# Performance work log

Hardware: AMD Instinct MI355X
Metric: run time of the kernel (lower is better)

Reference implementation:

```python
import jax, jax.numpy as jnp
import numpy as np

B, S, D, E, K = 4, 4096, 1024, 8, 2


def setup_inputs() -> dict:
    key = jax.random.key(0)
    k0, k1, k2 = jax.random.split(key, 3)
    return {
        "x": jax.random.normal(k0, (B, S, D), dtype=jnp.float32),
        "gate_w": jax.random.normal(k1, (E, D), dtype=jnp.float32) * 0.02,   # torch Linear weight [out,in]
        "gate_b": jnp.zeros((E,), dtype=jnp.float32),
        "expert_w": jax.random.normal(k2, (E, D, D), dtype=jnp.float32) * 0.02,  # [E, out, in]
        "expert_b": jnp.zeros((E, D), dtype=jnp.float32),
    }


def reference(x, gate_w, gate_b, expert_w, expert_b):
    b, s, d = x.shape
    h = x.reshape(-1, d)                                   # [T, D], T = b*s
    # Router: gate linear -> softmax (float32) -> top-k -> renormalize
    router_logits = h @ gate_w.T + gate_b                  # [T, E]
    probs = jax.nn.softmax(router_logits.astype(jnp.float32), axis=-1)
    router_weights, selected_experts = jax.lax.top_k(probs, K)  # [T, K]
    router_weights = router_weights / router_weights.sum(axis=-1, keepdims=True)
    router_weights = router_weights.astype(h.dtype)
    # Combine weights per (token, expert): sum of top-k weights routed to each expert
    cw = (jax.nn.one_hot(selected_experts, E, dtype=h.dtype)
          * router_weights[..., None]).sum(axis=1)         # [T, E]
    # Dense-equivalent of gather-linear-scatter: every expert on every token,
    # then weighted combine (mathematically identical to the per-expert loop).
    expert_out = jnp.einsum('td,eod->teo', h, expert_w) + expert_b[None]  # [T, E, D]
    out = jnp.einsum('te,teo->to', cw, expert_out)         # [T, D]
    return out.reshape(b, s, d), router_logits, selected_experts
```

## Files before the change

### kernel.cpp

```cpp
#include <hip/hip_runtime.h>
#include <hip/hip_bf16.h>

#define T_TOK 16384
#define D_DIM 1024
#define E_EXP 8
#define NPAIR 28

#define BM 128
#define BN 64
#define BK 64

#define CNT_STRIDE 64

typedef __attribute__((ext_vector_type(4))) float f32x4;
typedef __attribute__((ext_vector_type(2))) float f32x2;
typedef __attribute__((ext_vector_type(8))) short bf16x8;
typedef __attribute__((ext_vector_type(4))) unsigned short u16x4;

static __device__ __forceinline__ unsigned short f2bf(float f) {
    unsigned int u = __float_as_uint(f);
    unsigned int r = 0x7FFFu + ((u >> 16) & 1u);
    return (unsigned short)((u + r) >> 16);
}

#define GLOAD_LDS16(gp, lp) \
    __builtin_amdgcn_global_load_lds( \
        (const __attribute__((address_space(1))) void*)(gp), \
        (__attribute__((address_space(3))) void*)(lp), 16, 0, 0)

#define RTOK 64
#define RBLK 256
#define CBLK 128
__global__ __launch_bounds__(512) void fused_router_kernel(
    const float* __restrict__ x, const float* __restrict__ gate_w,
    const float* __restrict__ gate_b, float* __restrict__ out_logits,
    float* __restrict__ out_sel, int* __restrict__ counts,
    int* __restrict__ pair_token, f32x2* __restrict__ pair_w,
    unsigned short* __restrict__ xbf,
    const float* __restrict__ expert_w, unsigned short* __restrict__ wbf) {
    const int tid = threadIdx.x;
    if (blockIdx.x >= RBLK) {
        const int b = blockIdx.x - RBLK;
        const int n4 = (E_EXP * D_DIM * D_DIM) / 4;
        for (int i = b * 512 + tid; i < n4; i += CBLK * 512) {
            f32x4 v = ((const f32x4*)expert_w)[i];
            u16x4 p;
            p[0] = f2bf(v[0]); p[1] = f2bf(v[1]); p[2] = f2bf(v[2]); p[3] = f2bf(v[3]);
            ((u16x4*)wbf)[i] = p;
        }
        return;
    }
    __shared__ float gw[E_EXP][D_DIM];
    __shared__ float gb_s[E_EXP];
    __shared__ float logits_s[RTOK][E_EXP];
    __shared__ int   cnt_local[NPAIR];
    __shared__ int   gbase[NPAIR];
    __shared__ int   ent_p[RTOK];
    __shared__ int   ent_pos[RTOK];
    __shared__ f32x2 ent_w[RTOK];

    for (int i = tid; i < E_EXP * D_DIM; i += 512) gw[0][i] = gate_w[i];
    if (tid < E_EXP) gb_s[tid] = gate_b[tid];
    if (tid < NPAIR) cnt_local[tid] = 0;
    __syncthreads();

    const int lane = tid & 63, wv = tid >> 6;
    for (int j = 0; j < RTOK / 8; ++j) {
        const int jt = wv * (RTOK / 8) + j;
        const int t = blockIdx.x * RTOK + jt;
        const float* xrow = x + (size_t)t * D_DIM;
        unsigned short* xbrow = xbf + (size_t)t * D_DIM;
        float acc[E_EXP] = {};
        #pragma unroll
        for (int c = 0; c < 4; ++c) {
            const int col = c * 256 + lane * 4;
            f32x4 xv = *(const f32x4*)(xrow + col);
            u16x4 pk;
            pk[0] = f2bf(xv[0]); pk[1] = f2bf(xv[1]); pk[2] = f2bf(xv[2]); pk[3] = f2bf(xv[3]);
            *(u16x4*)(xbrow + col) = pk;
            #pragma unroll
            for (int e = 0; e < E_EXP; ++e) {
                f32x4 gv = *(const f32x4*)(&gw[e][col]);
                acc[e] += xv[0] * gv[0] + xv[1] * gv[1] + xv[2] * gv[2] + xv[3] * gv[3];
            }
        }
        #pragma unroll
        for (int e = 0; e < E_EXP; ++e) {
            float v = acc[e];
            #pragma unroll
            for (int off = 32; off > 0; off >>= 1) v += __shfl_xor(v, off, 64);
            acc[e] = v;
        }
        if (lane == 0) {
            #pragma unroll
            for (int e = 0; e < E_EXP; ++e) logits_s[jt][e] = acc[e] + gb_s[e];
        }
    }
    __syncthreads();
    if (tid < RTOK) {
        const int t = blockIdx.x * RTOK + tid;
        float l[E_EXP], p[E_EXP];
        float m = -1e30f;
        #pragma unroll
        for (int e = 0; e < E_EXP; ++e) { l[e] = logits_s[tid][e]; m = fmaxf(m, l[e]); }
        float s = 0.f;
        #pragma unroll
        for (int e = 0; e < E_EXP; ++e) { p[e] = expf(l[e] - m); s += p[e]; }
        #pragma unroll
        for (int e = 0; e < E_EXP; ++e) p[e] /= s;
        int e0 = 0; float p0 = p[0];
        #pragma unroll
        for (int e = 1; e < E_EXP; ++e) if (p[e] > p0) { p0 = p[e]; e0 = e; }
        int e1 = -1; float p1 = -1e30f;
        #pragma unroll
        for (int e = 0; e < E_EXP; ++e) if (e != e0 && p[e] > p1) { p1 = p[e]; e1 = e; }
        float denom = p0 + p1;
        float w0 = p0 / denom, w1 = p1 / denom;
        out_sel[t * 2 + 0] = (float)e0;
        out_sel[t * 2 + 1] = (float)e1;
        int lo = min(e0, e1), hi = max(e0, e1);
        float wl = (e0 < e1) ? w0 : w1;
        float wh = (e0 < e1) ? w1 : w0;
        int pp = (lo * (15 - lo)) / 2 + (hi - lo - 1);
        int pos = atomicAdd(&cnt_local[pp], 1);
        ent_p[tid] = pp; ent_pos[tid] = pos;
        f32x2 wv2; wv2[0] = wl; wv2[1] = wh;
        ent_w[tid] = wv2;
    }
    __syncthreads();
    if (tid < NPAIR) gbase[tid] = atomicAdd(&counts[tid * CNT_STRIDE], cnt_local[tid]);
    if (tid < RTOK * E_EXP / 4) {
        f32x4 v = ((const f32x4*)&logits_s[0][0])[tid];
        ((f32x4*)(out_logits + (size_t)blockIdx.x * RTOK * E_EXP))[tid] = v;
    }
    __syncthreads();
    if (tid < RTOK) {
        int pp = ent_p[tid];
        int pos = gbase[pp] + ent_pos[tid];
        pair_token[pp * T_TOK + pos] = blockIdx.x * RTOK + tid;
        pair_w[pp * T_TOK + pos] = ent_w[tid];
    }
}

__global__ __launch_bounds__(256, 2) void moe_gemm_kernel(
    const unsigned short* __restrict__ xbf, const unsigned short* __restrict__ wbf,
    const float* __restrict__ expert_b, const int* __restrict__ counts,
    const int* __restrict__ pair_token, const f32x2* __restrict__ pair_w,
    float* __restrict__ out) {
    const int flat = blockIdx.x;
    const int cls = flat & 7;
    const int nt  = (flat >> 3) & 15;
    const int sup = flat >> 7;

    __shared__ int hdr[5];
    const int tid = threadIdx.x;
    if (tid < 64) {
        int c = (tid < NPAIR) ? counts[tid * CNT_STRIDE] : 0;
        int ntp = (c + BM - 1) >> 7;
        int s = ntp;
        #pragma unroll
        for (int off = 1; off < 64; off <<= 1) {
            int v = __shfl_up(s, off, 64);
            if (tid >= off) s += v;
        }
        int excl = s - ntp;
        int ntot = __shfl(s, NPAIR - 1, 64);
        int chunk = (ntot + 7) >> 3;
        int gidx = cls * chunk + sup;
        bool valid = (sup < chunk) && (gidx < ntot);
        bool mine = valid && (tid < NPAIR) && (gidx >= excl) && (gidx < s);
        unsigned long long mb = __ballot(mine);
        int p = mb ? (__ffsll((long long)mb) - 1) : 0;
        int exclp = __shfl(excl, p, 64);
        int cp = __shfl(c, p, 64);
        if (tid == 0) {
            if (mb == 0) { hdr[0] = -1; }
            else {
                int lo = 0, q = p;
                while (q >= 7 - lo) { q -= 7 - lo; ++lo; }
                hdr[0] = lo; hdr[1] = lo + 1 + q;
                hdr[2] = (gidx - exclp) * BM; hdr[3] = cp; hdr[4] = p;
            }
        }
    }
    __syncthreads();
    const int lo = hdr[0];
    if (lo < 0) return;
    const int hi = hdr[1];
    const int m_base = hdr[2];
    const int cnt = hdr[3];
    const int p = hdr[4];
    const int n_base = nt * BN;

    __shared__ unsigned short As[BM * BK];
    __shared__ unsigned short B0s[BN * BK];
    __shared__ unsigned short B1s[BN * BK];
    __shared__ int tok_s[BM];
    __shared__ f32x2 w_s[BM];

    if (tid < BM) {
        int m = m_base + tid;
        int mc = (m < cnt) ? m : (cnt - 1);
        tok_s[tid] = pair_token[p * T_TOK + mc];
        w_s[tid]   = pair_w[p * T_TOK + mc];
    }
    __syncthreads();

    const int lane = tid & 63;
    const int w = tid >> 6;
    const int lr = lane & 15, lk = lane >> 4;
    const int wm = w >> 1, wn = w & 1;

    const int srow = lane >> 3;
    const int scol = 8 * ((lane & 7) ^ srow);
    const unsigned short* wb0 = wbf + ((size_t)lo << 20);
    const unsigned short* wb1 = wbf + ((size_t)hi << 20);
    const unsigned short* agp[4];
    const unsigned short* b0gp[2];
    const unsigned short* b1gp[2];
    int loffA[4], loffB[2];
    #pragma unroll
    for (int i = 0; i < 4; ++i) {
        int R = i * 32 + w * 8 + srow;
        agp[i]  = xbf + (size_t)tok_s[R] * D_DIM + scol;
        loffA[i] = (i * 32 + w * 8) * BK;
    }
    #pragma unroll
    for (int i = 0; i < 2; ++i) {
        int R = i * 32 + w * 8 + srow;
        b0gp[i] = wb0 + (size_t)(n_base + R) * D_DIM + scol;
        b1gp[i] = wb1 + (size_t)(n_base + R) * D_DIM + scol;
        loffB[i] = (i * 32 + w * 8) * BK;
    }

    f32x4 acc0[4][2] = {};
    f32x4 acc1[4][2] = {};

    for (int k0 = 0; k0 < D_DIM; k0 += BK) {
        #pragma unroll
        for (int i = 0; i < 4; ++i) GLOAD_LDS16(agp[i] + k0, &As[loffA[i]]);
        #pragma unroll
        for (int i = 0; i < 2; ++i) {
            GLOAD_LDS16(b0gp[i] + k0, &B0s[loffB[i]]);
            GLOAD_LDS16(b1gp[i] + k0, &B1s[loffB[i]]);
        }
        __syncthreads();
        #pragma unroll
        for (int kk = 0; kk < 2; ++kk) {
            bf16x8 a[4], b[2], c[2];
            #pragma unroll
            for (int m = 0; m < 4; ++m) {
                int R = wm * 64 + m * 16 + lr;
                int cb = (kk * 64 + lk * 16) ^ ((R & 7) << 4);
                a[m] = *(const bf16x8*)((const char*)As + R * 128 + cb);
            }
            #pragma unroll
            for (int n = 0; n < 2; ++n) {
                int R = wn * 32 + n * 16 + lr;
                int cb = (kk * 64 + lk * 16) ^ ((R & 7) << 4);
                b[n] = *(const bf16x8*)((const char*)B0s + R * 128 + cb);
                c[n] = *(const bf16x8*)((const char*)B1s + R * 128 + cb);
            }
            #pragma unroll
            for (int m = 0; m < 4; ++m)
                #pragma unroll
                for (int n = 0; n < 2; ++n)
                    acc0[m][n] = __builtin_amdgcn_mfma_f32_16x16x32_bf16(a[m], b[n], acc0[m][n], 0, 0, 0);
            #pragma unroll
            for (int m = 0; m < 4; ++m)
                #pragma unroll
                for (int n = 0; n < 2; ++n)
                    acc1[m][n] = __builtin_amdgcn_mfma_f32_16x16x32_bf16(a[m], c[n], acc1[m][n], 0, 0, 0);
        }
        __syncthreads();
    }

    float blo[2], bhi[2];
    #pragma unroll
    for (int n = 0; n < 2; ++n) {
        int gn = n_base + wn * 32 + n * 16 + lr;
        blo[n] = expert_b[lo * D_DIM + gn];
        bhi[n] = expert_b[hi * D_DIM + gn];
    }
    #pragma unroll
    for (int m = 0; m < 4; ++m) {
        #pragma unroll
        for (int j = 0; j < 4; ++j) {
            int mi = wm * 64 + m * 16 + lk * 4 + j;
            if (m_base + mi >= cnt) continue;
            int tk = tok_s[mi];
            f32x2 wgt = w_s[mi];
            size_t obase = (size_t)tk * D_DIM + n_base + wn * 32 + lr;
            #pragma unroll
            for (int n = 0; n < 2; ++n)
                out[obase + n * 16] = wgt[0] * (acc0[m][n][j] + blo[n])
                                    + wgt[1] * (acc1[m][n][j] + bhi[n]);
        }
    }
}

extern "C" void kernel_launch(void* const* d_in, const int* in_sizes, int n_in,
                              void* d_out, int out_size, void* d_ws, size_t ws_size,
                              hipStream_t stream) {
    const float* x        = (const float*)d_in[0];
    const float* gate_w   = (const float*)d_in[1];
    const float* gate_b   = (const float*)d_in[2];
    const float* expert_w = (const float*)d_in[3];
    const float* expert_b = (const float*)d_in[4];

    float* out        = (float*)d_out;
    float* out_logits = out + (size_t)T_TOK * D_DIM;
    float* out_sel    = out_logits + (size_t)T_TOK * E_EXP;

    char* ws = (char*)d_ws;
    unsigned short* wbf = (unsigned short*)ws;
    unsigned short* xbf = (unsigned short*)(ws + 16777216);
    size_t off = 50331648;
    int*   counts     = (int*)(ws + off);
    int*   pair_token = (int*)(ws + off + 16384);
    f32x2* pair_w     = (f32x2*)(ws + off + 16384 + 1835008);

    hipMemsetAsync(counts, 0, NPAIR * CNT_STRIDE * sizeof(int), stream);

    fused_router_kernel<<<RBLK + CBLK, 512, 0, stream>>>(
        x, gate_w, gate_b, out_logits, out_sel, counts, pair_token, pair_w,
        xbf, expert_w, wbf);
    moe_gemm_kernel<<<20 * 16 * 8, 256, 0, stream>>>(xbf, wbf, expert_b, counts,
                                                     pair_token, pair_w, out);
}
```

Measured before the change: 130.6 us.

## Load MFMA operands directly from global memory, dropping LDS staging

```diff
diff --git a/kernel.cpp b/kernel.cpp
--- a/kernel.cpp
+++ b/kernel.cpp
@@ -22,11 +22,6 @@
     unsigned int r = 0x7FFFu + ((u >> 16) & 1u);
     return (unsigned short)((u + r) >> 16);
 }
-
-#define GLOAD_LDS16(gp, lp) \
-    __builtin_amdgcn_global_load_lds( \
-        (const __attribute__((address_space(1))) void*)(gp), \
-        (__attribute__((address_space(3))) void*)(lp), 16, 0, 0)
 
 #define RTOK 64
 #define RBLK 256
@@ -153,6 +148,9 @@
     const int sup = flat >> 7;
 
     __shared__ int hdr[5];
+    __shared__ int tok_s[BM];
+    __shared__ f32x2 w_s[BM];
+
     const int tid = threadIdx.x;
     if (tid < 64) {
         int c = (tid < NPAIR) ? counts[tid * CNT_STRIDE] : 0;
@@ -192,12 +190,6 @@
     const int p = hdr[4];
     const int n_base = nt * BN;
 
-    __shared__ unsigned short As[BM * BK];
-    __shared__ unsigned short B0s[BN * BK];
-    __shared__ unsigned short B1s[BN * BK];
-    __shared__ int tok_s[BM];
-    __shared__ f32x2 w_s[BM];
-
     if (tid < BM) {
         int m = m_base + tid;
         int mc = (m < cnt) ? m : (cnt - 1);
@@ -211,68 +203,46 @@
     const int lr = lane & 15, lk = lane >> 4;
     const int wm = w >> 1, wn = w & 1;
 
-    const int srow = lane >> 3;
-    const int scol = 8 * ((lane & 7) ^ srow);
     const unsigned short* wb0 = wbf + ((size_t)lo << 20);
     const unsigned short* wb1 = wbf + ((size_t)hi << 20);
-    const unsigned short* agp[4];
-    const unsigned short* b0gp[2];
-    const unsigned short* b1gp[2];
-    int loffA[4], loffB[2];
+    const unsigned short* aB[4];
+    const unsigned short* b0B[2];
+    const unsigned short* b1B[2];
     #pragma unroll
-    for (int i = 0; i < 4; ++i) {
-        int R = i * 32 + w * 8 + srow;
-        agp[i]  = xbf + (size_t)tok_s[R] * D_DIM + scol;
-        loffA[i] = (i * 32 + w * 8) * BK;
+    for (int m = 0; m < 4; ++m) {
+        int row = wm * 64 + m * 16 + lr;
+        aB[m] = xbf + (size_t)tok_s[row] * D_DIM + lk * 8;
     }
     #pragma unroll
-    for (int i = 0; i < 2; ++i) {
-        int R = i * 32 + w * 8 + srow;
-        b0gp[i] = wb0 + (size_t)(n_base + R) * D_DIM + scol;
-        b1gp[i] = wb1 + (size_t)(n_base + R) * D_DIM + scol;
-        loffB[i] = (i * 32 + w * 8) * BK;
+    for (int n = 0; n < 2; ++n) {
+        int row = n_base + wn * 32 + n * 16 + lr;
+        b0B[n] = wb0 + (size_t)row * D_DIM + lk * 8;
+        b1B[n] = wb1 + (size_t)row * D_DIM + lk * 8;
     }
 
     f32x4 acc0[4][2] = {};
     f32x4 acc1[4][2] = {};
 
-    for (int k0 = 0; k0 < D_DIM; k0 += BK) {
-        #pragma unroll
-        for (int i = 0; i < 4; ++i) GLOAD_LDS16(agp[i] + k0, &As[loffA[i]]);
-        #pragma unroll
-        for (int i = 0; i < 2; ++i) {
-            GLOAD_LDS16(b0gp[i] + k0, &B0s[loffB[i]]);
-            GLOAD_LDS16(b1gp[i] + k0, &B1s[loffB[i]]);
-        }
-        __syncthreads();
-        #pragma unroll
-        for (int kk = 0; kk < 2; ++kk) {
-            bf16x8 a[4], b[2], c[2];
-            #pragma unroll
-            for (int m = 0; m < 4; ++m) {
-                int R = wm * 64 + m * 16 + lr;
-                int cb = (kk * 64 + lk * 16) ^ ((R & 7) << 4);
-                a[m] = *(const bf16x8*)((const char*)As + R * 128 + cb);
-            }
-            #pragma unroll
-            for (int n = 0; n < 2; ++n) {
-                int R = wn * 32 + n * 16 + lr;
-                int cb = (kk * 64 + lk * 16) ^ ((R & 7) << 4);
-                b[n] = *(const bf16x8*)((const char*)B0s + R * 128 + cb);
-                c[n] = *(const bf16x8*)((const char*)B1s + R * 128 + cb);
-            }
-            #pragma unroll
-            for (int m = 0; m < 4; ++m)
-                #pragma unroll
-                for (int n = 0; n < 2; ++n)
-                    acc0[m][n] = __builtin_amdgcn_mfma_f32_16x16x32_bf16(a[m], b[n], acc0[m][n], 0, 0, 0);
-            #pragma unroll
-            for (int m = 0; m < 4; ++m)
-                #pragma unroll
-                for (int n = 0; n < 2; ++n)
-                    acc1[m][n] = __builtin_amdgcn_mfma_f32_16x16x32_bf16(a[m], c[n], acc1[m][n], 0, 0, 0);
-        }
-        __syncthreads();
+    #pragma unroll 4
+    for (int k0 = 0; k0 < D_DIM; k0 += 32) {
+        bf16x8 a[4], b[2], c[2];
+        #pragma unroll
+        for (int m = 0; m < 4; ++m) a[m] = *(const bf16x8*)(aB[m] + k0);
+        #pragma unroll
+        for (int n = 0; n < 2; ++n) {
+            b[n] = *(const bf16x8*)(b0B[n] + k0);
+            c[n] = *(const bf16x8*)(b1B[n] + k0);
+        }
+        #pragma unroll
+        for (int m = 0; m < 4; ++m)
+            #pragma unroll
+            for (int n = 0; n < 2; ++n)
+                acc0[m][n] = __builtin_amdgcn_mfma_f32_16x16x32_bf16(a[m], b[n], acc0[m][n], 0, 0, 0);
+        #pragma unroll
+        for (int m = 0; m < 4; ++m)
+            #pragma unroll
+            for (int n = 0; n < 2; ++n)
+                acc1[m][n] = __builtin_amdgcn_mfma_f32_16x16x32_bf16(a[m], c[n], acc1[m][n], 0, 0, 0);
     }
 
     float blo[2], bhi[2];
```

New measurement: 302.8 us. 2.32x slower.
